# Performance work log

Hardware: AMD Instinct MI355X
Metric: run time of the kernel (lower is better)

Reference implementation:

```python
import jax, jax.numpy as jnp
import numpy as np

B, S, D, H = 2, 2048, 1024, 16
DK = D // H

def setup_inputs() -> dict:
    key = jax.random.key(0)
    ks = jax.random.split(key, 8)
    q = jax.random.normal(ks[0], (B, S, D), dtype=jnp.float32)
    k = jax.random.normal(ks[1], (B, S, D), dtype=jnp.float32)
    v = jax.random.normal(ks[2], (B, S, D), dtype=jnp.float32)
    # causal mask [B, S, S]; masked_fill where mask == 0
    mask = jnp.broadcast_to(jnp.tril(jnp.ones((S, S), dtype=jnp.int32)), (B, S, S))
    sc = 1.0 / np.sqrt(D)
    w_q = jax.random.normal(ks[3], (D, D), dtype=jnp.float32) * sc
    w_k = jax.random.normal(ks[4], (D, D), dtype=jnp.float32) * sc
    w_v = jax.random.normal(ks[5], (D, D), dtype=jnp.float32) * sc
    w_o = jax.random.normal(ks[6], (D, D), dtype=jnp.float32) * sc
    b_o = jnp.zeros((D,), dtype=jnp.float32)
    return {"query": q, "key": k, "value": v, "mask": mask,
            "w_q": w_q, "w_k": w_k, "w_v": w_v, "w_o": w_o, "b_o": b_o}

def reference(query, key, value, mask, w_q, w_k, w_v, w_o, b_o):
    # torch nn.Linear: y = x @ W.T
    def split_heads(x):
        return x.reshape(B, S, H, DK).transpose(0, 2, 1, 3)  # [B,H,S,DK]
    Q = split_heads(query @ w_q.T)
    K = split_heads(key @ w_k.T)
    V = split_heads(value @ w_v.T)
    scores = jnp.einsum('bhsd,bhtd->bhst', Q, K) / np.sqrt(DK)  # [B,H,S,S]
    m = mask[:, None, :, :]  # broadcast over heads
    scores = jnp.where(m == 0, jnp.float32(-1e9), scores)
    attn = jax.nn.softmax(scores, axis=-1)
    # dropout is identity in eval mode
    out = jnp.einsum('bhst,bhtd->bhsd', attn, V)  # [B,H,S,DK]
    out = out.transpose(0, 2, 1, 3).reshape(B, S, D)
    out = out @ w_o.T + b_o
    return (out, attn)
```

## Files before the change

### kernel.cpp

```cpp
#include <hip/hip_runtime.h>
#include <hip/hip_bf16.h>

#define S_LEN 2048
#define DMODEL 1024
#define NHEAD 16
#define DKH 64
#define NBATCH 2
#define NBH (NBATCH * NHEAD)
#define MROWS (NBATCH * S_LEN)
#define C1 0.18033688011112042f
#define C2 28.853900817779268f

typedef short bf16x8 __attribute__((ext_vector_type(8)));
typedef float f32x16 __attribute__((ext_vector_type(16)));
typedef float f32x4 __attribute__((ext_vector_type(4)));

typedef __attribute__((address_space(3))) void lds_void;
typedef __attribute__((address_space(1))) const void gbl_void;

__device__ __forceinline__ ushort f2bf(float f) {
  __hip_bfloat16 h = __float2bfloat16(f);
  union { __hip_bfloat16 h; ushort u; } c; c.h = h; return c.u;
}

__device__ __forceinline__ uint pack2(float a, float b) {
  float2 t; t.x = a; t.y = b;
  __hip_bfloat162 h = __float22bfloat162_rn(t);
  union { __hip_bfloat162 h; uint u; } c; c.h = h; return c.u;
}

__device__ __forceinline__ float bf2f(ushort u) {
  union { float f; uint u; } c; c.u = ((uint)u) << 16; return c.f;
}

__device__ __forceinline__ void gld16(void* lds, const void* g) {
  __builtin_amdgcn_global_load_lds((gbl_void*)(uintptr_t)g,
                                   (lds_void*)(uintptr_t)lds, 16, 0, 0);
}

__device__ __forceinline__ void gload_tile128(char* lds, const ushort* src, int strideE,
                                              int wid, int lane) {
#pragma unroll
  for (int j = 0; j < 4; j++) {
    int r = wid * 32 + j * 8 + (lane >> 3);
    int c = lane & 7;
    const char* g = (const char*)(src + (size_t)r * strideE) + ((c ^ (r & 7)) << 4);
    gld16(lds + wid * 4096 + j * 1024, g);
  }
}

__device__ __forceinline__ bf16x8 lds_frag(const char* base, int row, int kbyte) {
  int byte = row * 128 + kbyte;
  byte ^= (row & 7) << 4;
  return *(const bf16x8*)(base + byte);
}

__device__ __forceinline__ void tile_load_regs(const ushort* src, int srcStride,
                                               int tid, uint4& a, uint4& b) {
  int r = tid >> 2, cb = (tid & 3) * 32;
  const char* s = (const char*)(src + (size_t)r * srcStride) + cb;
  a = *(const uint4*)s;
  b = *(const uint4*)(s + 16);
}

__device__ __forceinline__ void tile_write_lds(char* dst, int tid,
                                               const uint4& a, const uint4& b) {
  int r = tid >> 2, cb = (tid & 3) * 32;
  int base = r * 128 + cb;
  int sw = (r & 7) << 4;
  *(uint4*)(dst + (base ^ sw)) = a;
  *(uint4*)(dst + ((base + 16) ^ sw)) = b;
}

__global__ __launch_bounds__(256) void cvt_kernel(
    const float* __restrict__ s0, ushort* __restrict__ d0,
    const float* __restrict__ s1, ushort* __restrict__ d1,
    const float* __restrict__ s2, ushort* __restrict__ d2,
    const float* __restrict__ s3, ushort* __restrict__ d3,
    const float* __restrict__ s4, ushort* __restrict__ d4,
    const float* __restrict__ s5, ushort* __restrict__ d5,
    const float* __restrict__ s6, ushort* __restrict__ d6) {
  const float* src; ushort* dst; int n;
  switch (blockIdx.y) {
    case 0: src = s0; dst = d0; n = MROWS * DMODEL; break;
    case 1: src = s1; dst = d1; n = MROWS * DMODEL; break;
    case 2: src = s2; dst = d2; n = MROWS * DMODEL; break;
    case 3: src = s3; dst = d3; n = DMODEL * DMODEL; break;
    case 4: src = s4; dst = d4; n = DMODEL * DMODEL; break;
    case 5: src = s5; dst = d5; n = DMODEL * DMODEL; break;
    default: src = s6; dst = d6; n = DMODEL * DMODEL; break;
  }
  for (size_t i = ((size_t)blockIdx.x * 256 + threadIdx.x) * 8; i < (size_t)n;
       i += (size_t)gridDim.x * 256 * 8) {
    float4 a = *(const float4*)(src + i);
    float4 b = *(const float4*)(src + i + 4);
    uint4 o = { pack2(a.x, a.y), pack2(a.z, a.w), pack2(b.x, b.y), pack2(b.z, b.w) };
    *(uint4*)(dst + i) = o;
  }
}

__global__ __launch_bounds__(256) void proj_kernel(
    const ushort* __restrict__ Xq, const ushort* __restrict__ Wq, ushort* __restrict__ Oq,
    const ushort* __restrict__ Xk, const ushort* __restrict__ Wk, ushort* __restrict__ Ok,
    const ushort* __restrict__ Xv, const ushort* __restrict__ Wv, ushort* __restrict__ Ov) {
  __shared__ char smem[34816];
  char* Xt = smem;
  char* Wt = smem + 16384;
  const ushort* X; const ushort* W; ushort* outH;
  if (blockIdx.z == 0)      { X = Xq; W = Wq; outH = Oq; }
  else if (blockIdx.z == 1) { X = Xk; W = Wk; outH = Ok; }
  else                      { X = Xv; W = Wv; outH = Ov; }

  int bm = blockIdx.x, bn = blockIdx.y;
  int tid = threadIdx.x;
  int lane = tid & 63, wid = tid >> 6;
  int l31 = lane & 31, hi = lane >> 5;
  int wr = wid >> 1, wc = wid & 1;
  f32x16 acc[2][2] = {};

  for (int kt = 0; kt < 1024; kt += 64) {
    __syncthreads();
    gload_tile128(Xt, X + (size_t)bm * 128 * 1024 + kt, 1024, wid, lane);
    gload_tile128(Wt, W + (size_t)bn * 128 * 1024 + kt, 1024, wid, lane);
    __syncthreads();
#pragma unroll
    for (int kk = 0; kk < 4; kk++) {
      bf16x8 a0 = lds_frag(Xt, 64 * wr + l31,      kk * 32 + hi * 16);
      bf16x8 a1 = lds_frag(Xt, 64 * wr + 32 + l31, kk * 32 + hi * 16);
      bf16x8 b0 = lds_frag(Wt, 64 * wc + l31,      kk * 32 + hi * 16);
      bf16x8 b1 = lds_frag(Wt, 64 * wc + 32 + l31, kk * 32 + hi * 16);
      acc[0][0] = __builtin_amdgcn_mfma_f32_32x32x16_bf16(a0, b0, acc[0][0], 0, 0, 0);
      acc[0][1] = __builtin_amdgcn_mfma_f32_32x32x16_bf16(a0, b1, acc[0][1], 0, 0, 0);
      acc[1][0] = __builtin_amdgcn_mfma_f32_32x32x16_bf16(a1, b0, acc[1][0], 0, 0, 0);
      acc[1][1] = __builtin_amdgcn_mfma_f32_32x32x16_bf16(a1, b1, acc[1][1], 0, 0, 0);
    }
  }
  __syncthreads();
  if (blockIdx.z != 2) {
    ushort (*ot)[136] = (ushort (*)[136])smem;
#pragma unroll
    for (int mi = 0; mi < 2; mi++)
#pragma unroll
      for (int ni = 0; ni < 2; ni++) {
        int col = wc * 64 + ni * 32 + l31;
#pragma unroll
        for (int rr = 0; rr < 16; rr++) {
          int row = wr * 64 + mi * 32 + (rr & 3) + 8 * (rr >> 2) + 4 * hi;
          ot[row][col] = f2bf(acc[mi][ni][rr]);
        }
      }
    __syncthreads();
    int r2 = tid >> 1, half = tid & 1;
    int m = bm * 128 + r2, b = m >> 11, s = m & 2047;
    int h = bn * 2 + half;
    ushort* dst = outH + ((size_t)(b * NHEAD + h) * S_LEN + s) * DKH;
    const ushort* srow = &ot[r2][half * 64];
#pragma unroll
    for (int j = 0; j < 8; j++)
      *(uint4*)(dst + j * 8) = *(const uint4*)(srow + j * 8);
  } else {
    ushort (*otT)[136] = (ushort (*)[136])smem;
#pragma unroll
    for (int mi = 0; mi < 2; mi++)
#pragma unroll
      for (int ni = 0; ni < 2; ni++) {
        int col = wc * 64 + ni * 32 + l31;
#pragma unroll
        for (int rr = 0; rr < 16; rr++) {
          int row = wr * 64 + mi * 32 + (rr & 3) + 8 * (rr >> 2) + 4 * hi;
          otT[col][row] = f2bf(acc[mi][ni][rr]);
        }
      }
    __syncthreads();
    int col2 = tid >> 1, sh = (tid & 1) * 64;
    int b = bm >> 4, s0 = (bm & 15) * 128;
    int h = bn * 2 + (col2 >> 6), d = col2 & 63;
    ushort* dst = outH + ((size_t)(b * NHEAD + h) * DKH + d) * S_LEN + s0 + sh;
    const ushort* srow = &otT[col2][sh];
#pragma unroll
    for (int j = 0; j < 8; j++)
      *(uint4*)(dst + j * 8) = *(const uint4*)(srow + j * 8);
  }
}

__global__ __launch_bounds__(256) void outproj_kernel(const ushort* __restrict__ A,
                                                      const ushort* __restrict__ W,
                                                      const float* __restrict__ bias,
                                                      float* __restrict__ out) {
  __shared__ char smem[33792];
  char* Xt = smem;
  char* Wt = smem + 16384;
  int bm = blockIdx.x, bn = blockIdx.y;
  int tid = threadIdx.x;
  int lane = tid & 63, wid = tid >> 6;
  int l31 = lane & 31, hi = lane >> 5;
  int wr = wid >> 1, wc = wid & 1;
  f32x16 acc[2][2] = {};

  for (int kt = 0; kt < 1024; kt += 64) {
    __syncthreads();
    gload_tile128(Xt, A + (size_t)bm * 128 * 1024 + kt, 1024, wid, lane);
    gload_tile128(Wt, W + (size_t)bn * 128 * 1024 + kt, 1024, wid, lane);
    __syncthreads();
#pragma unroll
    for (int kk = 0; kk < 4; kk++) {
      bf16x8 a0 = lds_frag(Xt, 64 * wr + l31,      kk * 32 + hi * 16);
      bf16x8 a1 = lds_frag(Xt, 64 * wr + 32 + l31, kk * 32 + hi * 16);
      bf16x8 b0 = lds_frag(Wt, 64 * wc + l31,      kk * 32 + hi * 16);
      bf16x8 b1 = lds_frag(Wt, 64 * wc + 32 + l31, kk * 32 + hi * 16);
      acc[0][0] = __builtin_amdgcn_mfma_f32_32x32x16_bf16(a0, b0, acc[0][0], 0, 0, 0);
      acc[0][1] = __builtin_amdgcn_mfma_f32_32x32x16_bf16(a0, b1, acc[0][1], 0, 0, 0);
      acc[1][0] = __builtin_amdgcn_mfma_f32_32x32x16_bf16(a1, b0, acc[1][0], 0, 0, 0);
      acc[1][1] = __builtin_amdgcn_mfma_f32_32x32x16_bf16(a1, b1, acc[1][1], 0, 0, 0);
    }
  }
  for (int mi = 0; mi < 2; mi++) {
    __syncthreads();
    {
      float (*of)[132] = (float (*)[132])smem;
#pragma unroll
      for (int ni = 0; ni < 2; ni++) {
        int col = wc * 64 + ni * 32 + l31;
        float bv = bias[bn * 128 + col];
#pragma unroll
        for (int rr = 0; rr < 16; rr++) {
          int lrow = wr * 32 + (rr & 3) + 8 * (rr >> 2) + 4 * hi;
          of[lrow][col] = acc[mi][ni][rr] + bv;
        }
      }
    }
    __syncthreads();
    {
      float (*of)[132] = (float (*)[132])smem;
      int lr = tid >> 2, ck = (tid & 3) * 32;
      int m = bm * 128 + (lr >> 5) * 64 + mi * 32 + (lr & 31);
      float* dst = out + (size_t)m * DMODEL + bn * 128 + ck;
#pragma unroll
      for (int j = 0; j < 8; j++)
        *(float4*)(dst + j * 4) = *(const float4*)(&of[lr][ck] + j * 4);
    }
  }
}

__global__ __launch_bounds__(256) void attn_kernel(const ushort* __restrict__ Qh,
                                                   const ushort* __restrict__ Kh,
                                                   const ushort* __restrict__ VTh,
                                                   float* __restrict__ attn,
                                                   ushort* __restrict__ Oc) {
  __shared__ char smem[41728];
  char* Kt0 = smem;
  char* Kt1 = smem + 8192;
  char* Vt0 = smem + 16384;
  char* Vt1 = smem + 24576;
  char* Pt  = smem + 32768;
  float* lpart = (float*)(smem + 40960);
  float* lfin  = lpart + 128;

  int bid = blockIdx.x;
  int xcd = bid & 7, idx = bid >> 3;
  int bh = (idx & 3) * 8 + xcd;
  int qx = idx >> 2;

  int tid = threadIdx.x;
  int wid = tid >> 6, lane = tid & 63;
  int l31 = lane & 31, hi = lane >> 5;
  int wr = wid >> 1, wc = wid & 1;

  const ushort* Kbase = Kh  + (size_t)bh * S_LEN * DKH;
  const ushort* Vbase = VTh + (size_t)bh * DKH * S_LEN;

  for (int half = 0; half < 2; half++) {
    int qb = half ? (31 - qx) : qx;
    int nt = qb + 1;
    int qg = qb * 64 + 32 * wc + l31;

    __syncthreads();

    bf16x8 qf[4];
    {
      const ushort* qrow = Qh + ((size_t)bh * S_LEN + qb * 64 + 32 * wc + l31) * DKH + hi * 8;
#pragma unroll
      for (int kk = 0; kk < 4; kk++) qf[kk] = *(const bf16x8*)(qrow + kk * 16);
    }

    {
      int zstart = nt * 64;
      f32x4 z4 = {0.f, 0.f, 0.f, 0.f};
      for (int rg = 0; rg < 4; rg++) {
        float* dst = attn + ((size_t)bh * S_LEN + qb * 64 + (tid >> 4) + rg * 16) * S_LEN;
        for (int c = zstart + (tid & 15) * 4; c < S_LEN; c += 64)
          *(f32x4*)(dst + c) = z4;
      }
    }

    {
      uint4 a, b;
      tile_load_regs(Kbase, DKH, tid, a, b);
      tile_write_lds(Kt0, tid, a, b);
    }
    __syncthreads();
    float l_ln = 0.f;
    for (int kb = 0; kb < nt; kb++) {
      char* cur = (kb & 1) ? Kt1 : Kt0;
      char* nxt = (kb & 1) ? Kt0 : Kt1;
      uint4 pa, pb;
      bool pre = (kb + 1 < nt);
      if (pre) tile_load_regs(Kbase + (size_t)(kb + 1) * 64 * DKH, DKH, tid, pa, pb);
      f32x16 sacc = {};
      __builtin_amdgcn_s_setprio(1);
#pragma unroll
      for (int kk = 0; kk < 4; kk++) {
        bf16x8 a = lds_frag(cur, 32 * wr + l31, kk * 32 + hi * 16);
        sacc = __builtin_amdgcn_mfma_f32_32x32x16_bf16(a, qf[kk], sacc, 0, 0, 0);
      }
      __builtin_amdgcn_s_setprio(0);
      int kbase_g = kb * 64 + 32 * wr + 4 * hi;
      if (kb == qb) {
#pragma unroll
        for (int rr = 0; rr < 16; rr++) {
          int kg = kbase_g + (rr & 3) + 8 * (rr >> 2);
          float fs = fminf(fmaf(sacc[rr], C1, -C2), 86.f);
          l_ln += (kg > qg) ? 0.f : exp2f(fs);
        }
      } else {
#pragma unroll
        for (int rr = 0; rr < 16; rr++)
          l_ln += exp2f(fminf(fmaf(sacc[rr], C1, -C2), 86.f));
      }
      if (pre) tile_write_lds(nxt, tid, pa, pb);
      __syncthreads();
    }
    {
      float L = l_ln + __shfl_xor(l_ln, 32);
      if (lane < 32) lpart[wid * 32 + l31] = L;
    }
    __syncthreads();
    if (tid < 64) {
      int wcq = tid >> 5, qq = tid & 31;
      lfin[tid] = 1.0f / (lpart[wcq * 32 + qq] + lpart[(wcq + 2) * 32 + qq]);
    }
    __syncthreads();
    float liq = lfin[32 * wc + l31];

    f32x16 oacc = {};
    {
      uint4 ka, kb2, va, vb2;
      tile_load_regs(Kbase, DKH, tid, ka, kb2);
      tile_load_regs(Vbase, S_LEN, tid, va, vb2);
      tile_write_lds(Kt0, tid, ka, kb2);
      tile_write_lds(Vt0, tid, va, vb2);
    }
    __syncthreads();
    for (int kb = 0; kb < nt; kb++) {
      char* kcur = (kb & 1) ? Kt1 : Kt0;
      char* knxt = (kb & 1) ? Kt0 : Kt1;
      char* vcur = (kb & 1) ? Vt1 : Vt0;
      char* vnxt = (kb & 1) ? Vt0 : Vt1;
      uint4 ka, kb2, va, vb2;
      bool pre = (kb + 1 < nt);
      if (pre) {
        tile_load_regs(Kbase + (size_t)(kb + 1) * 64 * DKH, DKH, tid, ka, kb2);
        tile_load_regs(Vbase + (size_t)(kb + 1) * 64, S_LEN, tid, va, vb2);
      }
      f32x16 sacc = {};
      __builtin_amdgcn_s_setprio(1);
#pragma unroll
      for (int kk = 0; kk < 4; kk++) {
        bf16x8 a = lds_frag(kcur, 32 * wr + l31, kk * 32 + hi * 16);
        sacc = __builtin_amdgcn_mfma_f32_32x32x16_bf16(a, qf[kk], sacc, 0, 0, 0);
      }
      __builtin_amdgcn_s_setprio(0);
      int kbase_g = kb * 64 + 32 * wr + 4 * hi;
      float pv[16];
      if (kb == qb) {
#pragma unroll
        for (int rr = 0; rr < 16; rr++) {
          int kg = kbase_g + (rr & 3) + 8 * (rr >> 2);
          float fs = fminf(fmaf(sacc[rr], C1, -C2), 86.f);
          pv[rr] = (kg > qg) ? 0.f : exp2f(fs) * liq;
        }
      } else {
#pragma unroll
        for (int rr = 0; rr < 16; rr++)
          pv[rr] = exp2f(fminf(fmaf(sacc[rr], C1, -C2), 86.f)) * liq;
      }
      {
        int row = 32 * wc + l31;
        int sw = (row & 7) << 4;
#pragma unroll
        for (int g = 0; g < 4; g++) {
          uint2 pb2 = { pack2(pv[4 * g], pv[4 * g + 1]), pack2(pv[4 * g + 2], pv[4 * g + 3]) };
          int byte = row * 128 + (32 * wr + 8 * g + 4 * hi) * 2;
          *(uint2*)(Pt + (byte ^ sw)) = pb2;
        }
      }
      __syncthreads();
      __builtin_amdgcn_s_setprio(1);
#pragma unroll
      for (int kk = 0; kk < 4; kk++) {
        bf16x8 a = lds_frag(Pt,   32 * wr + l31, kk * 32 + hi * 16);
        bf16x8 b = lds_frag(vcur, 32 * wc + l31, kk * 32 + hi * 16);
        oacc = __builtin_amdgcn_mfma_f32_32x32x16_bf16(a, b, oacc, 0, 0, 0);
      }
      __builtin_amdgcn_s_setprio(0);
      {
        const float* abase = attn + ((size_t)bh * S_LEN + qb * 64) * S_LEN + kb * 64;
#pragma unroll
        for (int r = 0; r < 4; r++) {
          int row = r * 16 + (tid >> 4);
          int colf = (tid & 15) * 4;
          int byte = (row * 128 + colf * 2) ^ ((row & 7) << 4);
          ushort4 u = *(const ushort4*)(Pt + byte);
          f32x4 f = { bf2f(u.x), bf2f(u.y), bf2f(u.z), bf2f(u.w) };
          *(f32x4*)((float*)abase + (size_t)row * S_LEN + colf) = f;
        }
      }
      if (pre) {
        tile_write_lds(knxt, tid, ka, kb2);
        tile_write_lds(vnxt, tid, va, vb2);
      }
      __syncthreads();
    }

    float* Os = (float*)smem;
    {
      int col = 32 * wc + l31;
#pragma unroll
      for (int rr = 0; rr < 16; rr++) {
        int row = 32 * wr + (rr & 3) + 8 * (rr >> 2) + 4 * hi;
        Os[row * 64 + col] = oacc[rr];
      }
    }
    __syncthreads();
    {
      int b = bh >> 4, h = bh & 15;
      int r = tid >> 2, c0 = (tid & 3) * 16;
      uint w[8];
#pragma unroll
      for (int j = 0; j < 8; j++)
        w[j] = pack2(Os[r * 64 + c0 + 2 * j], Os[r * 64 + c0 + 2 * j + 1]);
      ushort* dst = Oc + ((size_t)(b * S_LEN + qb * 64 + r)) * DMODEL + h * 64 + c0;
      *(uint4*)dst = *(uint4*)&w[0];
      *(uint4*)(dst + 8) = *(uint4*)&w[4];
    }
  }
}

extern "C" void kernel_launch(void* const* d_in, const int* in_sizes, int n_in,
                              void* d_out, int out_size, void* d_ws, size_t ws_size,
                              hipStream_t stream) {
  (void)in_sizes; (void)n_in; (void)out_size; (void)ws_size;
  const float* q  = (const float*)d_in[0];
  const float* k  = (const float*)d_in[1];
  const float* v  = (const float*)d_in[2];
  const float* wq = (const float*)d_in[4];
  const float* wk = (const float*)d_in[5];
  const float* wv = (const float*)d_in[6];
  const float* wo = (const float*)d_in[7];
  const float* bo = (const float*)d_in[8];

  float* out  = (float*)d_out;
  float* attn = out + (size_t)MROWS * DMODEL;

  char* ws = (char*)d_ws;
  const size_t XSZ = (size_t)MROWS * DMODEL * sizeof(ushort);
  const size_t WSZ = (size_t)DMODEL * DMODEL * sizeof(ushort);
  ushort* Xq  = (ushort*)(ws);
  ushort* Xk  = (ushort*)(ws + XSZ);
  ushort* Xv  = (ushort*)(ws + 2 * XSZ);
  ushort* Wqb = (ushort*)(ws + 3 * XSZ);
  ushort* Wkb = (ushort*)(ws + 3 * XSZ + WSZ);
  ushort* Wvb = (ushort*)(ws + 3 * XSZ + 2 * WSZ);
  ushort* Wob = (ushort*)(ws + 3 * XSZ + 3 * WSZ);
  char*   ws2 = ws + 3 * XSZ + 4 * WSZ;
  ushort* Qh  = (ushort*)(ws2);
  ushort* Kh  = (ushort*)(ws2 + XSZ);
  ushort* VTh = (ushort*)(ws2 + 2 * XSZ);
  ushort* Oc  = (ushort*)(ws2 + 3 * XSZ);

  dim3 blk(256);
  hipLaunchKernelGGL(cvt_kernel, dim3(512, 7), blk, 0, stream,
                     q, Xq, k, Xk, v, Xv, wq, Wqb, wk, Wkb, wv, Wvb, wo, Wob);
  hipLaunchKernelGGL(proj_kernel, dim3(32, 8, 3), blk, 0, stream,
                     Xq, Wqb, Qh, Xk, Wkb, Kh, Xv, Wvb, VTh);
  hipLaunchKernelGGL(attn_kernel, dim3(512), blk, 0, stream, Qh, Kh, VTh, attn, Oc);
  hipLaunchKernelGGL(outproj_kernel, dim3(32, 8), blk, 0, stream, Oc, Wob, bo, out);
}
```

Before: 249.7 us.

## Split attention into one query block per workgroup and interleave masked-zero writes

Each workgroup now processes a single query block (heaviest first) instead of a balanced pair, doubling the grid. The zero-fill of the masked upper triangle is redistributed so a block with qb writes the complementary row's masked tiles inside its PV loop, overlapping stores with compute. The P tile is double-buffered, allowing the K-tile prefetch write to move before the barrier and reducing sync stalls. LDS usage grows, which may lower occupancy, and per-block Q loads and launch overhead increase.

Measured after the change: 292.3 us. 1.17x slower.

```diff
diff --git a/kernel.cpp b/kernel.cpp
--- a/kernel.cpp
+++ b/kernel.cpp
@@ -247,19 +247,21 @@
                                                    const ushort* __restrict__ VTh,
                                                    float* __restrict__ attn,
                                                    ushort* __restrict__ Oc) {
-  __shared__ char smem[41728];
+  __shared__ char smem[49920];
   char* Kt0 = smem;
   char* Kt1 = smem + 8192;
   char* Vt0 = smem + 16384;
   char* Vt1 = smem + 24576;
-  char* Pt  = smem + 32768;
-  float* lpart = (float*)(smem + 40960);
+  char* Pt0 = smem + 32768;
+  char* Pt1 = smem + 40960;
+  float* lpart = (float*)(smem + 49152);
   float* lfin  = lpart + 128;
 
   int bid = blockIdx.x;
   int xcd = bid & 7, idx = bid >> 3;
   int bh = (idx & 3) * 8 + xcd;
-  int qx = idx >> 2;
+  int qb = 31 - (idx >> 2);
+  int nt = qb + 1;
 
   int tid = threadIdx.x;
   int wid = tid >> 6, lane = tid & 63;
@@ -268,181 +270,173 @@
 
   const ushort* Kbase = Kh  + (size_t)bh * S_LEN * DKH;
   const ushort* Vbase = VTh + (size_t)bh * DKH * S_LEN;
-
-  for (int half = 0; half < 2; half++) {
-    int qb = half ? (31 - qx) : qx;
-    int nt = qb + 1;
-    int qg = qb * 64 + 32 * wc + l31;
-
-    __syncthreads();
-
-    bf16x8 qf[4];
+  int qg = qb * 64 + 32 * wc + l31;
+
+  bf16x8 qf[4];
+  {
+    const ushort* qrow = Qh + ((size_t)bh * S_LEN + qb * 64 + 32 * wc + l31) * DKH + hi * 8;
+#pragma unroll
+    for (int kk = 0; kk < 4; kk++) qf[kk] = *(const bf16x8*)(qrow + kk * 16);
+  }
+
+  {
+    uint4 a, b;
+    tile_load_regs(Kbase, DKH, tid, a, b);
+    tile_write_lds(Kt0, tid, a, b);
+  }
+  __syncthreads();
+  float l_ln = 0.f;
+  for (int kb = 0; kb < nt; kb++) {
+    char* cur = (kb & 1) ? Kt1 : Kt0;
+    char* nxt = (kb & 1) ? Kt0 : Kt1;
+    uint4 pa, pb;
+    bool pre = (kb + 1 < nt);
+    if (pre) tile_load_regs(Kbase + (size_t)(kb + 1) * 64 * DKH, DKH, tid, pa, pb);
+    f32x16 sacc = {};
+    __builtin_amdgcn_s_setprio(1);
+#pragma unroll
+    for (int kk = 0; kk < 4; kk++) {
+      bf16x8 a = lds_frag(cur, 32 * wr + l31, kk * 32 + hi * 16);
+      sacc = __builtin_amdgcn_mfma_f32_32x32x16_bf16(a, qf[kk], sacc, 0, 0, 0);
+    }
+    __builtin_amdgcn_s_setprio(0);
+    int kbase_g = kb * 64 + 32 * wr + 4 * hi;
+    if (kb == qb) {
+#pragma unroll
+      for (int rr = 0; rr < 16; rr++) {
+        int kg = kbase_g + (rr & 3) + 8 * (rr >> 2);
+        float fs = fminf(fmaf(sacc[rr], C1, -C2), 86.f);
+        l_ln += (kg > qg) ? 0.f : exp2f(fs);
+      }
+    } else {
+#pragma unroll
+      for (int rr = 0; rr < 16; rr++)
+        l_ln += exp2f(fminf(fmaf(sacc[rr], C1, -C2), 86.f));
+    }
+    if (pre) tile_write_lds(nxt, tid, pa, pb);
+    __syncthreads();
+  }
+  {
+    float L = l_ln + __shfl_xor(l_ln, 32);
+    if (lane < 32) lpart[wid * 32 + l31] = L;
+  }
+  __syncthreads();
+  if (tid < 64) {
+    int wcq = tid >> 5, qq = tid & 31;
+    lfin[tid] = 1.0f / (lpart[wcq * 32 + qq] + lpart[(wcq + 2) * 32 + qq]);
+  }
+  __syncthreads();
+  float liq = lfin[32 * wc + l31];
+
+  f32x16 oacc = {};
+  {
+    uint4 ka, kb2, va, vb2;
+    tile_load_regs(Kbase, DKH, tid, ka, kb2);
+    tile_load_regs(Vbase, S_LEN, tid, va, vb2);
+    tile_write_lds(Kt0, tid, ka, kb2);
+    tile_write_lds(Vt0, tid, va, vb2);
+  }
+  __syncthreads();
+  int zr = 31 - qb;
+  float* zbase = attn + ((size_t)bh * S_LEN + zr * 64 + (tid >> 2)) * S_LEN + (tid & 3) * 16;
+  for (int kb = 0; kb < nt; kb++) {
+    char* kcur = (kb & 1) ? Kt1 : Kt0;
+    char* knxt = (kb & 1) ? Kt0 : Kt1;
+    char* pcur = (kb & 1) ? Pt1 : Pt0;
+    char* vcur = (kb & 1) ? Vt1 : Vt0;
+    char* vnxt = (kb & 1) ? Vt0 : Vt1;
+    uint4 ka, kb2, va, vb2;
+    bool pre = (kb + 1 < nt);
+    if (pre) {
+      tile_load_regs(Kbase + (size_t)(kb + 1) * 64 * DKH, DKH, tid, ka, kb2);
+      tile_load_regs(Vbase + (size_t)(kb + 1) * 64, S_LEN, tid, va, vb2);
+    }
+    f32x16 sacc = {};
+    __builtin_amdgcn_s_setprio(1);
+#pragma unroll
+    for (int kk = 0; kk < 4; kk++) {
+      bf16x8 a = lds_frag(kcur, 32 * wr + l31, kk * 32 + hi * 16);
+      sacc = __builtin_amdgcn_mfma_f32_32x32x16_bf16(a, qf[kk], sacc, 0, 0, 0);
+    }
+    __builtin_amdgcn_s_setprio(0);
+    int kbase_g = kb * 64 + 32 * wr + 4 * hi;
+    float pv[16];
+    if (kb == qb) {
+#pragma unroll
+      for (int rr = 0; rr < 16; rr++) {
+        int kg = kbase_g + (rr & 3) + 8 * (rr >> 2);
+        float fs = fminf(fmaf(sacc[rr], C1, -C2), 86.f);
+        pv[rr] = (kg > qg) ? 0.f : exp2f(fs) * liq;
+      }
+    } else {
+#pragma unroll
+      for (int rr = 0; rr < 16; rr++)
+        pv[rr] = exp2f(fminf(fmaf(sacc[rr], C1, -C2), 86.f)) * liq;
+    }
     {
-      const ushort* qrow = Qh + ((size_t)bh * S_LEN + qb * 64 + 32 * wc + l31) * DKH + hi * 8;
-#pragma unroll
-      for (int kk = 0; kk < 4; kk++) qf[kk] = *(const bf16x8*)(qrow + kk * 16);
-    }
-
+      int row = 32 * wc + l31;
+      int sw = (row & 7) << 4;
+#pragma unroll
+      for (int g = 0; g < 4; g++) {
+        uint2 pb2 = { pack2(pv[4 * g], pv[4 * g + 1]), pack2(pv[4 * g + 2], pv[4 * g + 3]) };
+        int byte = row * 128 + (32 * wr + 8 * g + 4 * hi) * 2;
+        *(uint2*)(pcur + (byte ^ sw)) = pb2;
+      }
+    }
+    if (pre) tile_write_lds(knxt, tid, ka, kb2);
+    __syncthreads();
+    __builtin_amdgcn_s_setprio(1);
+#pragma unroll
+    for (int kk = 0; kk < 4; kk++) {
+      bf16x8 a = lds_frag(pcur, 32 * wr + l31, kk * 32 + hi * 16);
+      bf16x8 b = lds_frag(vcur, 32 * wc + l31, kk * 32 + hi * 16);
+      oacc = __builtin_amdgcn_mfma_f32_32x32x16_bf16(a, b, oacc, 0, 0, 0);
+    }
+    __builtin_amdgcn_s_setprio(0);
     {
-      int zstart = nt * 64;
+      const float* abase = attn + ((size_t)bh * S_LEN + qb * 64) * S_LEN + kb * 64;
+#pragma unroll
+      for (int r = 0; r < 4; r++) {
+        int row = r * 16 + (tid >> 4);
+        int colf = (tid & 15) * 4;
+        int byte = (row * 128 + colf * 2) ^ ((row & 7) << 4);
+        ushort4 u = *(const ushort4*)(pcur + byte);
+        f32x4 f = { bf2f(u.x), bf2f(u.y), bf2f(u.z), bf2f(u.w) };
+        *(f32x4*)((float*)abase + (size_t)row * S_LEN + colf) = f;
+      }
+    }
+    if (pre) tile_write_lds(vnxt, tid, va, vb2);
+    if (kb < qb) {
+      float* zt = zbase + (size_t)(32 - qb + kb) * 64;
       f32x4 z4 = {0.f, 0.f, 0.f, 0.f};
-      for (int rg = 0; rg < 4; rg++) {
-        float* dst = attn + ((size_t)bh * S_LEN + qb * 64 + (tid >> 4) + rg * 16) * S_LEN;
-        for (int c = zstart + (tid & 15) * 4; c < S_LEN; c += 64)
-          *(f32x4*)(dst + c) = z4;
-      }
-    }
-
-    {
-      uint4 a, b;
-      tile_load_regs(Kbase, DKH, tid, a, b);
-      tile_write_lds(Kt0, tid, a, b);
-    }
-    __syncthreads();
-    float l_ln = 0.f;
-    for (int kb = 0; kb < nt; kb++) {
-      char* cur = (kb & 1) ? Kt1 : Kt0;
-      char* nxt = (kb & 1) ? Kt0 : Kt1;
-      uint4 pa, pb;
-      bool pre = (kb + 1 < nt);
-      if (pre) tile_load_regs(Kbase + (size_t)(kb + 1) * 64 * DKH, DKH, tid, pa, pb);
-      f32x16 sacc = {};
-      __builtin_amdgcn_s_setprio(1);
-#pragma unroll
-      for (int kk = 0; kk < 4; kk++) {
-        bf16x8 a = lds_frag(cur, 32 * wr + l31, kk * 32 + hi * 16);
-        sacc = __builtin_amdgcn_mfma_f32_32x32x16_bf16(a, qf[kk], sacc, 0, 0, 0);
-      }
-      __builtin_amdgcn_s_setprio(0);
-      int kbase_g = kb * 64 + 32 * wr + 4 * hi;
-      if (kb == qb) {
-#pragma unroll
-        for (int rr = 0; rr < 16; rr++) {
-          int kg = kbase_g + (rr & 3) + 8 * (rr >> 2);
-          float fs = fminf(fmaf(sacc[rr], C1, -C2), 86.f);
-          l_ln += (kg > qg) ? 0.f : exp2f(fs);
-        }
-      } else {
-#pragma unroll
-        for (int rr = 0; rr < 16; rr++)
-          l_ln += exp2f(fminf(fmaf(sacc[rr], C1, -C2), 86.f));
-      }
-      if (pre) tile_write_lds(nxt, tid, pa, pb);
-      __syncthreads();
-    }
-    {
-      float L = l_ln + __shfl_xor(l_ln, 32);
-      if (lane < 32) lpart[wid * 32 + l31] = L;
-    }
-    __syncthreads();
-    if (tid < 64) {
-      int wcq = tid >> 5, qq = tid & 31;
-      lfin[tid] = 1.0f / (lpart[wcq * 32 + qq] + lpart[(wcq + 2) * 32 + qq]);
-    }
-    __syncthreads();
-    float liq = lfin[32 * wc + l31];
-
-    f32x16 oacc = {};
-    {
-      uint4 ka, kb2, va, vb2;
-      tile_load_regs(Kbase, DKH, tid, ka, kb2);
-      tile_load_regs(Vbase, S_LEN, tid, va, vb2);
-      tile_write_lds(Kt0, tid, ka, kb2);
-      tile_write_lds(Vt0, tid, va, vb2);
-    }
-    __syncthreads();
-    for (int kb = 0; kb < nt; kb++) {
-      char* kcur = (kb & 1) ? Kt1 : Kt0;
-      char* knxt = (kb & 1) ? Kt0 : Kt1;
-      char* vcur = (kb & 1) ? Vt1 : Vt0;
-      char* vnxt = (kb & 1) ? Vt0 : Vt1;
-      uint4 ka, kb2, va, vb2;
-      bool pre = (kb + 1 < nt);
-      if (pre) {
-        tile_load_regs(Kbase + (size_t)(kb + 1) * 64 * DKH, DKH, tid, ka, kb2);
-        tile_load_regs(Vbase + (size_t)(kb + 1) * 64, S_LEN, tid, va, vb2);
-      }
-      f32x16 sacc = {};
-      __builtin_amdgcn_s_setprio(1);
-#pragma unroll
-      for (int kk = 0; kk < 4; kk++) {
-        bf16x8 a = lds_frag(kcur, 32 * wr + l31, kk * 32 + hi * 16);
-        sacc = __builtin_amdgcn_mfma_f32_32x32x16_bf16(a, qf[kk], sacc, 0, 0, 0);
-      }
-      __builtin_amdgcn_s_setprio(0);
-      int kbase_g = kb * 64 + 32 * wr + 4 * hi;
-      float pv[16];
-      if (kb == qb) {
-#pragma unroll
-        for (int rr = 0; rr < 16; rr++) {
-          int kg = kbase_g + (rr & 3) + 8 * (rr >> 2);
-          float fs = fminf(fmaf(sacc[rr], C1, -C2), 86.f);
-          pv[rr] = (kg > qg) ? 0.f : exp2f(fs) * liq;
-        }
-      } else {
-#pragma unroll
-        for (int rr = 0; rr < 16; rr++)
-          pv[rr] = exp2f(fminf(fmaf(sacc[rr], C1, -C2), 86.f)) * liq;
-      }
-      {
-        int row = 32 * wc + l31;
-        int sw = (row & 7) << 4;
-#pragma unroll
-        for (int g = 0; g < 4; g++) {
-          uint2 pb2 = { pack2(pv[4 * g], pv[4 * g + 1]), pack2(pv[4 * g + 2], pv[4 * g + 3]) };
-          int byte = row * 128 + (32 * wr + 8 * g + 4 * hi) * 2;
-          *(uint2*)(Pt + (byte ^ sw)) = pb2;
-        }
-      }
-      __syncthreads();
-      __builtin_amdgcn_s_setprio(1);
-#pragma unroll
-      for (int kk = 0; kk < 4; kk++) {
-        bf16x8 a = lds_frag(Pt,   32 * wr + l31, kk * 32 + hi * 16);
-        bf16x8 b = lds_frag(vcur, 32 * wc + l31, kk * 32 + hi * 16);
-        oacc = __builtin_amdgcn_mfma_f32_32x32x16_bf16(a, b, oacc, 0, 0, 0);
-      }
-      __builtin_amdgcn_s_setprio(0);
-      {
-        const float* abase = attn + ((size_t)bh * S_LEN + qb * 64) * S_LEN + kb * 64;
-#pragma unroll
-        for (int r = 0; r < 4; r++) {
-          int row = r * 16 + (tid >> 4);
-          int colf = (tid & 15) * 4;
-          int byte = (row * 128 + colf * 2) ^ ((row & 7) << 4);
-          ushort4 u = *(const ushort4*)(Pt + byte);
-          f32x4 f = { bf2f(u.x), bf2f(u.y), bf2f(u.z), bf2f(u.w) };
-          *(f32x4*)((float*)abase + (size_t)row * S_LEN + colf) = f;
-        }
-      }
-      if (pre) {
-        tile_write_lds(knxt, tid, ka, kb2);
-        tile_write_lds(vnxt, tid, va, vb2);
-      }
-      __syncthreads();
-    }
-
-    float* Os = (float*)smem;
-    {
-      int col = 32 * wc + l31;
-#pragma unroll
-      for (int rr = 0; rr < 16; rr++) {
-        int row = 32 * wr + (rr & 3) + 8 * (rr >> 2) + 4 * hi;
-        Os[row * 64 + col] = oacc[rr];
-      }
-    }
-    __syncthreads();
-    {
-      int b = bh >> 4, h = bh & 15;
-      int r = tid >> 2, c0 = (tid & 3) * 16;
-      uint w[8];
-#pragma unroll
-      for (int j = 0; j < 8; j++)
-        w[j] = pack2(Os[r * 64 + c0 + 2 * j], Os[r * 64 + c0 + 2 * j + 1]);
-      ushort* dst = Oc + ((size_t)(b * S_LEN + qb * 64 + r)) * DMODEL + h * 64 + c0;
-      *(uint4*)dst = *(uint4*)&w[0];
-      *(uint4*)(dst + 8) = *(uint4*)&w[4];
-    }
+      *(f32x4*)(zt)      = z4;
+      *(f32x4*)(zt + 4)  = z4;
+      *(f32x4*)(zt + 8)  = z4;
+      *(f32x4*)(zt + 12) = z4;
+    }
+  }
+
+  __syncthreads();
+  float* Os = (float*)smem;
+  {
+    int col = 32 * wc + l31;
+#pragma unroll
+    for (int rr = 0; rr < 16; rr++) {
+      int row = 32 * wr + (rr & 3) + 8 * (rr >> 2) + 4 * hi;
+      Os[row * 64 + col] = oacc[rr];
+    }
+  }
+  __syncthreads();
+  {
+    int b = bh >> 4, h = bh & 15;
+    int r = tid >> 2, c0 = (tid & 3) * 16;
+    uint w[8];
+#pragma unroll
+    for (int j = 0; j < 8; j++)
+      w[j] = pack2(Os[r * 64 + c0 + 2 * j], Os[r * 64 + c0 + 2 * j + 1]);
+    ushort* dst = Oc + ((size_t)(b * S_LEN + qb * 64 + r)) * DMODEL + h * 64 + c0;
+    *(uint4*)dst = *(uint4*)&w[0];
+    *(uint4*)(dst + 8) = *(uint4*)&w[4];
   }
 }
 
@@ -483,6 +477,6 @@
                      q, Xq, k, Xk, v, Xv, wq, Wqb, wk, Wkb, wv, Wvb, wo, Wob);
   hipLaunchKernelGGL(proj_kernel, dim3(32, 8, 3), blk, 0, stream,
                      Xq, Wqb, Qh, Xk, Wkb, Kh, Xv, Wvb, VTh);
-  hipLaunchKernelGGL(attn_kernel, dim3(512), blk, 0, stream, Qh, Kh, VTh, attn, Oc);
+  hipLaunchKernelGGL(attn_kernel, dim3(1024), blk, 0, stream, Qh, Kh, VTh, attn, Oc);
   hipLaunchKernelGGL(outproj_kernel, dim3(32, 8), blk, 0, stream, Oc, Wob, bo, out);
 }
```
